# Kernel tuning notes

Hardware: AMD Instinct MI355X
Metric: run time of the kernel (lower is better)

Reference implementation:

```python
import jax, jax.numpy as jnp
import numpy as np

TEMPERATURE = 0.5
B, D = 4096, 256


def setup_inputs() -> dict:
    key = jax.random.key(0)
    k1, k2 = jax.random.split(key)
    emb_i = jax.random.normal(k1, (B, D), dtype=jnp.float32)
    emb_j = jax.random.normal(k2, (B, D), dtype=jnp.float32)
    return {"emb_i": emb_i, "emb_j": emb_j}


def reference(emb_i, emb_j):
    # NT-Xent (SimCLR) loss, vectorized version of the per-sample python loop.
    n = emb_i.shape[0]
    eps = 1e-12
    z_i = emb_i / jnp.maximum(jnp.linalg.norm(emb_i, axis=1, keepdims=True), eps)
    z_j = emb_j / jnp.maximum(jnp.linalg.norm(emb_j, axis=1, keepdims=True), eps)
    reps = jnp.concatenate([z_i, z_j], axis=0)               # [2N, D], unit rows
    # cosine similarity of unit vectors == dot product
    sim = reps @ reps.T                                       # [2N, 2N]
    exp_sim = jnp.exp(sim / TEMPERATURE)
    # denominator for row i: sum over k != i of exp(sim[i,k]/T)
    denom = jnp.sum(exp_sim, axis=1) - jnp.diagonal(exp_sim)  # [2N]
    # positive-pair sims: sim[k, k+N] and sim[k+N, k]
    pos = jnp.concatenate([jnp.diagonal(sim[:n, n:]), jnp.diagonal(sim[n:, :n])])
    # l_ij = log(exp(pos/T) / denom) = pos/T - log(denom)
    loss_terms = pos / TEMPERATURE - jnp.log(denom)
    return (1.0 / (2 * n)) * jnp.sum(loss_terms)
```

## Files before the change

kernel.cpp:

```cpp
#include <hip/hip_runtime.h>
#include <math.h>


#define NROWS 8192
#define NHALF 4096
#define DIM   256
#define BM    128
#define BN    128
#define BK    64
#define NCB   (NROWS / BN)
#define NTRI  (NCB * (NCB + 1) / 2)

#define SCALE    1.69864344f
#define POSMUL   1.38629436f

typedef __attribute__((ext_vector_type(8))) short bf16x8;
typedef __attribute__((ext_vector_type(4))) float f32x4;

#if __has_builtin(__builtin_amdgcn_exp2f)
#define EXP2(x) __builtin_amdgcn_exp2f(x)
#else
#define EXP2(x) __expf((x) * 0.69314718f)
#endif

static __device__ __forceinline__ unsigned short f2bf(float x) {
  unsigned int u = __float_as_uint(x);
  unsigned int r = (u + 0x7FFFu + ((u >> 16) & 1u)) >> 16;
  return (unsigned short)r;
}

__global__ __launch_bounds__(256) void normalize_kernel(
    const float* __restrict__ emb_i, const float* __restrict__ emb_j,
    unsigned short* __restrict__ zb, float* __restrict__ out) {
  if (blockIdx.x == 0 && threadIdx.x == 0) out[0] = 0.f;
  int w = threadIdx.x >> 6, lane = threadIdx.x & 63;
  int row = blockIdx.x * 4 + w;
  const float* src = (row < NHALF) ? (emb_i + (size_t)row * DIM)
                                   : (emb_j + (size_t)(row - NHALF) * DIM);
  float4 v = ((const float4*)src)[lane];
  float ss = v.x * v.x + v.y * v.y + v.z * v.z + v.w * v.w;
  #pragma unroll
  for (int off = 32; off; off >>= 1) ss += __shfl_down(ss, off, 64);
  float total = __shfl(ss, 0, 64);
  float inv = SCALE / fmaxf(sqrtf(total), 1e-12f);
  ushort4 o;
  o.x = f2bf(v.x * inv); o.y = f2bf(v.y * inv);
  o.z = f2bf(v.z * inv); o.w = f2bf(v.w * inv);
  ((ushort4*)&zb[(size_t)row * DIM])[lane] = o;
}

__global__ __launch_bounds__(256) void denom_kernel(
    const unsigned short* __restrict__ zb, float* __restrict__ denomP,
    float* __restrict__ posv) {
  __shared__ __attribute__((aligned(16))) unsigned short As[16 * 512];
  __shared__ __attribute__((aligned(16))) unsigned short Bs[16 * 512];

  int t = blockIdx.x;
  int by = (int)((sqrtf(8.0f * (float)t + 1.0f) - 1.0f) * 0.5f);
  while ((by + 1) * (by + 2) / 2 <= t) ++by;
  while (by * (by + 1) / 2 > t) --by;
  int bx = t - by * (by + 1) / 2;

  const int tid = threadIdx.x;
  const int w = tid >> 6;
  const int lane = tid & 63;
  const int wr = w >> 1, wc = w & 1;
  const int quad = lane >> 4;
  const int m16 = lane & 15;
  const int row0 = bx * BM;
  const int col0 = by * BN;

  f32x4 acc[4][4];
  #pragma unroll
  for (int i = 0; i < 4; ++i)
    #pragma unroll
    for (int j = 0; j < 4; ++j) {
      f32x4 z4 = {0.f, 0.f, 0.f, 0.f};
      acc[i][j] = z4;
    }

  for (int kc = 0; kc < DIM; kc += BK) {
    #pragma unroll
    for (int t4 = 0; t4 < 4; ++t4) {
      int ra = w * 4 + t4;
      int grow = (ra >> 1) * 16 + m16;
      int gk = kc + (ra & 1) * 32 + quad * 8;
      __builtin_amdgcn_global_load_lds(
          (const __attribute__((address_space(1))) unsigned int*)
              &zb[(size_t)(row0 + grow) * DIM + gk],
          (__attribute__((address_space(3))) unsigned int*)&As[ra * 512],
          16, 0, 0);
      __builtin_amdgcn_global_load_lds(
          (const __attribute__((address_space(1))) unsigned int*)
              &zb[(size_t)(col0 + grow) * DIM + gk],
          (__attribute__((address_space(3))) unsigned int*)&Bs[ra * 512],
          16, 0, 0);
    }
    __syncthreads();

    #pragma unroll
    for (int ks = 0; ks < BK; ks += 32) {
      const int kst = ks >> 5;
      bf16x8 af[4], bfr[4];
      #pragma unroll
      for (int i = 0; i < 4; ++i)
        af[i] = *(const bf16x8*)&As[(wr * 8 + i * 2 + kst) * 512 + lane * 8];
      #pragma unroll
      for (int j = 0; j < 4; ++j)
        bfr[j] = *(const bf16x8*)&Bs[(wc * 8 + j * 2 + kst) * 512 + lane * 8];
      #pragma unroll
      for (int i = 0; i < 4; ++i)
        #pragma unroll
        for (int j = 0; j < 4; ++j)
          acc[i][j] = __builtin_amdgcn_mfma_f32_16x16x32_bf16(
              af[i], bfr[j], acc[i][j], 0, 0, 0);
    }
    __syncthreads();
  }

  if (col0 - row0 == NHALF) {
    #pragma unroll
    for (int i = 0; i < 4; ++i)
      #pragma unroll
      for (int j = 0; j < 4; ++j) {
        int gcol = col0 + wc * 64 + j * 16 + m16;
        #pragma unroll
        for (int r = 0; r < 4; ++r) {
          int grow = row0 + wr * 64 + i * 16 + quad * 4 + r;
          if (gcol - grow == NHALF) posv[grow] = acc[i][j][r];
        }
      }
  }

  float rs[4][4];
  float cs[4] = {0.f, 0.f, 0.f, 0.f};
  #pragma unroll
  for (int i = 0; i < 4; ++i)
    #pragma unroll
    for (int r = 0; r < 4; ++r) rs[i][r] = 0.f;

  #pragma unroll
  for (int i = 0; i < 4; ++i)
    #pragma unroll
    for (int j = 0; j < 4; ++j) {
      int gcol = col0 + wc * 64 + j * 16 + m16;
      #pragma unroll
      for (int r = 0; r < 4; ++r) {
        int grow = row0 + wr * 64 + i * 16 + quad * 4 + r;
        float e = (grow == gcol) ? 0.f : EXP2(acc[i][j][r]);
        rs[i][r] += e;
        cs[j] += e;
      }
    }

  float* red = (float*)As;

  #pragma unroll
  for (int i = 0; i < 4; ++i)
    #pragma unroll
    for (int r = 0; r < 4; ++r) {
      float v = rs[i][r];
      v += __shfl_xor(v, 1, 16);
      v += __shfl_xor(v, 2, 16);
      v += __shfl_xor(v, 4, 16);
      v += __shfl_xor(v, 8, 16);
      if (m16 == 0) red[wc * 128 + wr * 64 + i * 16 + quad * 4 + r] = v;
    }
  #pragma unroll
  for (int j = 0; j < 4; ++j) {
    float v = cs[j];
    v += __shfl_xor(v, 16, 64);
    v += __shfl_xor(v, 32, 64);
    if (quad == 0) red[256 + wr * 128 + wc * 64 + j * 16 + m16] = v;
  }
  __syncthreads();

  if (tid < 128) {
    denomP[(size_t)by * NROWS + row0 + tid] = red[tid] + red[128 + tid];
  } else if (bx != by) {
    int c = tid - 128;
    denomP[(size_t)bx * NROWS + col0 + c] = red[256 + c] + red[384 + c];
  }
}

__global__ __launch_bounds__(256) void reduce_kernel(
    const float* __restrict__ denomP, const float* __restrict__ posv,
    float* __restrict__ out) {
  int tid = threadIdx.x;
  int r = blockIdx.x * 256 + tid;
  float s = 0.f;
  #pragma unroll 8
  for (int b = 0; b < NCB; ++b) s += denomP[(size_t)b * NROWS + r];
  float v = -logf(s);
  if (r < NHALF) v += POSMUL * posv[r];
  #pragma unroll
  for (int off = 32; off; off >>= 1) v += __shfl_down(v, off, 64);
  __shared__ float s4[4];
  if ((tid & 63) == 0) s4[tid >> 6] = v;
  __syncthreads();
  if (tid == 0)
    atomicAdd(out, (s4[0] + s4[1] + s4[2] + s4[3]) * (1.0f / 8192.0f));
}

extern "C" void kernel_launch(void* const* d_in, const int* in_sizes, int n_in,
                              void* d_out, int out_size, void* d_ws,
                              size_t ws_size, hipStream_t stream) {
  const float* emb_i = (const float*)d_in[0];
  const float* emb_j = (const float*)d_in[1];
  unsigned short* zb = (unsigned short*)d_ws;
  float* denomP = (float*)(zb + (size_t)NROWS * DIM);
  float* posv = denomP + (size_t)NCB * NROWS;
  float* out = (float*)d_out;

  normalize_kernel<<<NROWS / 4, 256, 0, stream>>>(emb_i, emb_j, zb, out);
  denom_kernel<<<NTRI, 256, 0, stream>>>(zb, denomP, posv);
  reduce_kernel<<<NROWS / 256, 256, 0, stream>>>(denomP, posv, out);
}
```

Measured before the change: 116.8 us.

## Fuse final reduction into denom kernel via atomic ticket, double K tile

Removes the separate reduce kernel launch: each denom block takes an atomic ticket, and the last 32 blocks to finish spin until every tile has landed, then do the per-row log-sum and the atomic accumulation into the output. BK is doubled to 128, so the 256-wide K dimension is loaded in two stages instead of four, halving barrier round trips at the cost of twice the LDS per block. Diagonal tiles get a specialised epilogue that skips the column sums and the mask check on off-diagonal tiles. The spin-wait depends on all other blocks making progress and adds a serial tail in the last blocks.

```diff
diff --git a/kernel.cpp b/kernel.cpp
--- a/kernel.cpp
+++ b/kernel.cpp
@@ -7,9 +7,10 @@
 #define DIM   256
 #define BM    128
 #define BN    128
-#define BK    64
+#define BK    128
 #define NCB   (NROWS / BN)
 #define NTRI  (NCB * (NCB + 1) / 2)
+#define NRED  32
 
 #define SCALE    1.69864344f
 #define POSMUL   1.38629436f
@@ -31,8 +32,9 @@
 
 __global__ __launch_bounds__(256) void normalize_kernel(
     const float* __restrict__ emb_i, const float* __restrict__ emb_j,
-    unsigned short* __restrict__ zb, float* __restrict__ out) {
-  if (blockIdx.x == 0 && threadIdx.x == 0) out[0] = 0.f;
+    unsigned short* __restrict__ zb, float* __restrict__ out,
+    int* __restrict__ cnt) {
+  if (blockIdx.x == 0 && threadIdx.x == 0) { out[0] = 0.f; cnt[0] = 0; }
   int w = threadIdx.x >> 6, lane = threadIdx.x & 63;
   int row = blockIdx.x * 4 + w;
   const float* src = (row < NHALF) ? (emb_i + (size_t)row * DIM)
@@ -51,9 +53,9 @@
 
 __global__ __launch_bounds__(256) void denom_kernel(
     const unsigned short* __restrict__ zb, float* __restrict__ denomP,
-    float* __restrict__ posv) {
-  __shared__ __attribute__((aligned(16))) unsigned short As[16 * 512];
-  __shared__ __attribute__((aligned(16))) unsigned short Bs[16 * 512];
+    float* __restrict__ posv, int* __restrict__ cnt, float* __restrict__ out) {
+  __shared__ __attribute__((aligned(16))) unsigned short As[32 * 512];
+  __shared__ __attribute__((aligned(16))) unsigned short Bs[32 * 512];
 
   int t = blockIdx.x;
   int by = (int)((sqrtf(8.0f * (float)t + 1.0f) - 1.0f) * 0.5f);
@@ -81,10 +83,10 @@
 
   for (int kc = 0; kc < DIM; kc += BK) {
     #pragma unroll
-    for (int t4 = 0; t4 < 4; ++t4) {
-      int ra = w * 4 + t4;
-      int grow = (ra >> 1) * 16 + m16;
-      int gk = kc + (ra & 1) * 32 + quad * 8;
+    for (int t8 = 0; t8 < 8; ++t8) {
+      int ra = w * 8 + t8;
+      int grow = (ra >> 2) * 16 + m16;
+      int gk = kc + (ra & 3) * 32 + quad * 8;
       __builtin_amdgcn_global_load_lds(
           (const __attribute__((address_space(1))) unsigned int*)
               &zb[(size_t)(row0 + grow) * DIM + gk],
@@ -99,15 +101,14 @@
     __syncthreads();
 
     #pragma unroll
-    for (int ks = 0; ks < BK; ks += 32) {
-      const int kst = ks >> 5;
+    for (int kst = 0; kst < 4; ++kst) {
       bf16x8 af[4], bfr[4];
       #pragma unroll
       for (int i = 0; i < 4; ++i)
-        af[i] = *(const bf16x8*)&As[(wr * 8 + i * 2 + kst) * 512 + lane * 8];
+        af[i] = *(const bf16x8*)&As[(wr * 16 + i * 4 + kst) * 512 + lane * 8];
       #pragma unroll
       for (int j = 0; j < 4; ++j)
-        bfr[j] = *(const bf16x8*)&Bs[(wc * 8 + j * 2 + kst) * 512 + lane * 8];
+        bfr[j] = *(const bf16x8*)&Bs[(wc * 16 + j * 4 + kst) * 512 + lane * 8];
       #pragma unroll
       for (int i = 0; i < 4; ++i)
         #pragma unroll
@@ -132,62 +133,101 @@
       }
   }
 
-  float rs[4][4];
-  float cs[4] = {0.f, 0.f, 0.f, 0.f};
-  #pragma unroll
-  for (int i = 0; i < 4; ++i)
-    #pragma unroll
-    for (int r = 0; r < 4; ++r) rs[i][r] = 0.f;
-
-  #pragma unroll
-  for (int i = 0; i < 4; ++i)
+  float* red = (float*)As;
+
+  if (bx != by) {
+    float rs[4][4];
+    float cs[4] = {0.f, 0.f, 0.f, 0.f};
+    #pragma unroll
+    for (int i = 0; i < 4; ++i)
+      #pragma unroll
+      for (int r = 0; r < 4; ++r) rs[i][r] = 0.f;
+    #pragma unroll
+    for (int i = 0; i < 4; ++i)
+      #pragma unroll
+      for (int j = 0; j < 4; ++j)
+        #pragma unroll
+        for (int r = 0; r < 4; ++r) {
+          float e = EXP2(acc[i][j][r]);
+          rs[i][r] += e;
+          cs[j] += e;
+        }
+    #pragma unroll
+    for (int i = 0; i < 4; ++i)
+      #pragma unroll
+      for (int r = 0; r < 4; ++r) {
+        float v = rs[i][r];
+        v += __shfl_xor(v, 1, 16);
+        v += __shfl_xor(v, 2, 16);
+        v += __shfl_xor(v, 4, 16);
+        v += __shfl_xor(v, 8, 16);
+        if (m16 == 0) red[wc * 128 + wr * 64 + i * 16 + quad * 4 + r] = v;
+      }
     #pragma unroll
     for (int j = 0; j < 4; ++j) {
-      int gcol = col0 + wc * 64 + j * 16 + m16;
+      float v = cs[j];
+      v += __shfl_xor(v, 16, 64);
+      v += __shfl_xor(v, 32, 64);
+      if (quad == 0) red[256 + wr * 128 + wc * 64 + j * 16 + m16] = v;
+    }
+    __syncthreads();
+    if (tid < 128) {
+      denomP[(size_t)by * NROWS + row0 + tid] = red[tid] + red[128 + tid];
+    } else {
+      int c = tid - 128;
+      denomP[(size_t)bx * NROWS + col0 + c] = red[256 + c] + red[384 + c];
+    }
+  } else {
+    float rs[4][4];
+    #pragma unroll
+    for (int i = 0; i < 4; ++i)
+      #pragma unroll
+      for (int r = 0; r < 4; ++r) rs[i][r] = 0.f;
+    #pragma unroll
+    for (int i = 0; i < 4; ++i)
+      #pragma unroll
+      for (int j = 0; j < 4; ++j) {
+        int lcol = wc * 64 + j * 16 + m16;
+        #pragma unroll
+        for (int r = 0; r < 4; ++r) {
+          int lrow = wr * 64 + i * 16 + quad * 4 + r;
+          float e = (lrow == lcol) ? 0.f : EXP2(acc[i][j][r]);
+          rs[i][r] += e;
+        }
+      }
+    #pragma unroll
+    for (int i = 0; i < 4; ++i)
       #pragma unroll
       for (int r = 0; r < 4; ++r) {
-        int grow = row0 + wr * 64 + i * 16 + quad * 4 + r;
-        float e = (grow == gcol) ? 0.f : EXP2(acc[i][j][r]);
-        rs[i][r] += e;
-        cs[j] += e;
-      }
-    }
-
-  float* red = (float*)As;
-
-  #pragma unroll
-  for (int i = 0; i < 4; ++i)
-    #pragma unroll
-    for (int r = 0; r < 4; ++r) {
-      float v = rs[i][r];
-      v += __shfl_xor(v, 1, 16);
-      v += __shfl_xor(v, 2, 16);
-      v += __shfl_xor(v, 4, 16);
-      v += __shfl_xor(v, 8, 16);
-      if (m16 == 0) red[wc * 128 + wr * 64 + i * 16 + quad * 4 + r] = v;
-    }
-  #pragma unroll
-  for (int j = 0; j < 4; ++j) {
-    float v = cs[j];
-    v += __shfl_xor(v, 16, 64);
-    v += __shfl_xor(v, 32, 64);
-    if (quad == 0) red[256 + wr * 128 + wc * 64 + j * 16 + m16] = v;
-  }
+        float v = rs[i][r];
+        v += __shfl_xor(v, 1, 16);
+        v += __shfl_xor(v, 2, 16);
+        v += __shfl_xor(v, 4, 16);
+        v += __shfl_xor(v, 8, 16);
+        if (m16 == 0) red[wc * 128 + wr * 64 + i * 16 + quad * 4 + r] = v;
+      }
+    __syncthreads();
+    if (tid < 128)
+      denomP[(size_t)bx * NROWS + row0 + tid] = red[tid] + red[128 + tid];
+  }
+
+  __threadfence();
+  __shared__ int ticket_s;
+  if (tid == 0) ticket_s = atomicAdd(cnt, 1);
   __syncthreads();
-
-  if (tid < 128) {
-    denomP[(size_t)by * NROWS + row0 + tid] = red[tid] + red[128 + tid];
-  } else if (bx != by) {
-    int c = tid - 128;
-    denomP[(size_t)bx * NROWS + col0 + c] = red[256 + c] + red[384 + c];
-  }
-}
-
-__global__ __launch_bounds__(256) void reduce_kernel(
-    const float* __restrict__ denomP, const float* __restrict__ posv,
-    float* __restrict__ out) {
-  int tid = threadIdx.x;
-  int r = blockIdx.x * 256 + tid;
+  int ticket = ticket_s;
+  if (ticket < NTRI - NRED) return;
+  int slice = ticket - (NTRI - NRED);
+
+  if (tid == 0) {
+    while (__hip_atomic_load(cnt, __ATOMIC_ACQUIRE,
+                             __HIP_MEMORY_SCOPE_AGENT) < NTRI)
+      __builtin_amdgcn_s_sleep(8);
+  }
+  __syncthreads();
+  __threadfence();
+
+  int r = slice * 256 + tid;
   float s = 0.f;
   #pragma unroll 8
   for (int b = 0; b < NCB; ++b) s += denomP[(size_t)b * NROWS + r];
@@ -195,11 +235,10 @@
   if (r < NHALF) v += POSMUL * posv[r];
   #pragma unroll
   for (int off = 32; off; off >>= 1) v += __shfl_down(v, off, 64);
-  __shared__ float s4[4];
-  if ((tid & 63) == 0) s4[tid >> 6] = v;
+  if ((tid & 63) == 0) red[tid >> 6] = v;
   __syncthreads();
   if (tid == 0)
-    atomicAdd(out, (s4[0] + s4[1] + s4[2] + s4[3]) * (1.0f / 8192.0f));
+    atomicAdd(out, (red[0] + red[1] + red[2] + red[3]) * (1.0f / 8192.0f));
 }
 
 extern "C" void kernel_launch(void* const* d_in, const int* in_sizes, int n_in,
@@ -210,9 +249,9 @@
   unsigned short* zb = (unsigned short*)d_ws;
   float* denomP = (float*)(zb + (size_t)NROWS * DIM);
   float* posv = denomP + (size_t)NCB * NROWS;
+  int* cnt = (int*)(posv + NHALF);
   float* out = (float*)d_out;
 
-  normalize_kernel<<<NROWS / 4, 256, 0, stream>>>(emb_i, emb_j, zb, out);
-  denom_kernel<<<NTRI, 256, 0, stream>>>(zb, denomP, posv);
-  reduce_kernel<<<NROWS / 256, 256, 0, stream>>>(denomP, posv, out);
-}
+  normalize_kernel<<<NROWS / 4, 256, 0, stream>>>(emb_i, emb_j, zb, out, cnt);
+  denom_kernel<<<NTRI, 256, 0, stream>>>(zb, denomP, posv, cnt, out);
+}
```

Result: slower. 245.4 us (+110.1%).
